# Optimization experiments

Measured on AMD Instinct MI355X. Metric: run time of the kernel, lower is better.

The kernel has to match this reference:

```python
import jax, jax.numpy as jnp
import numpy as np

N_STEPS = 3  # fixed propagation depth standing in for the BFS-guided delta_st recursion


def setup_inputs() -> dict:
    key = jax.random.key(0)
    ks = jax.random.split(key, 12)
    n, d, E = 32, 96, 256
    f32 = jnp.float32
    rn = lambda k, s, sc: jax.random.normal(k, s, f32) * sc
    return {
        "node_embeddings": rn(ks[0], (n, d), 1.0),
        "edges": jax.random.randint(ks[1], (E, 2), 0, n, jnp.int32),
        "w1": rn(ks[2], (4, 4, 3), 0.3), "b1": jnp.full((4,), 0.01, f32),
        "w2": rn(ks[3], (4, 4, 3), 0.3), "b2": jnp.full((4,), 0.01, f32),
        "w3": rn(ks[4], (4, 4, 3), 0.3), "b3": jnp.full((4,), 0.01, f32),
        "fc1_w": rn(ks[5], (16, 128), 0.2), "fc1_b": jnp.full((128,), 0.01, f32),
        "fc2_w": rn(ks[6], (128, 256), 0.1), "fc2_b": jnp.full((256,), 0.01, f32),
        "fc3_w": rn(ks[7], (256, 128), 0.1), "fc3_b": jnp.full((128,), 0.01, f32),
        "fc4_w": rn(ks[8], (128, 1), 0.1), "fc4_b": jnp.full((1,), 0.01, f32),
    }


def _conv1d(x, w, b, stride):
    # x: [B, C, L], w: [O, I, K]
    y = jax.lax.conv_general_dilated(x, w, (stride,), 'VALID',
                                     dimension_numbers=('NCH', 'OIH', 'NCH'))
    return y + b[None, :, None]


def _maxpool2(x):
    return jax.lax.reduce_window(x, -jnp.inf, jax.lax.max, (1, 1, 2), (1, 1, 2), 'VALID')


def _conv_pool_stack(x, w1, b1, w2, b2, w3, b3,
                     fc1_w, fc1_b, fc2_w, fc2_b, fc3_w, fc3_b, fc4_w, fc4_b):
    # x: [B, 4, 96] -> [B]
    h = _maxpool2(jax.nn.relu(_conv1d(x, w1, b1, 2)))   # [B,4,23]
    h = _maxpool2(jax.nn.relu(_conv1d(h, w2, b2, 1)))   # [B,4,10]
    h = _maxpool2(jax.nn.relu(_conv1d(h, w3, b3, 1)))   # [B,4,4]
    h = h.reshape(h.shape[0], -1)                       # [B,16]
    h = jax.nn.relu(h @ fc1_w + fc1_b)
    h = jax.nn.relu(h @ fc2_w + fc2_b)
    h = jax.nn.relu(h @ fc3_w + fc3_b)
    return (h @ fc4_w + fc4_b)[:, 0]


def reference(node_embeddings, edges, w1, b1, w2, b2, w3, b3,
              fc1_w, fc1_b, fc2_w, fc2_b, fc3_w, fc3_b, fc4_w, fc4_b):
    n, d = node_embeddings.shape
    E = edges.shape[0]
    u_idx, v_idx = edges[:, 0], edges[:, 1]

    # All (s, t) node pairs, flattened: P = n*n (s == t masked out below).
    s_idx, t_idx = jnp.meshgrid(jnp.arange(n), jnp.arange(n), indexing='ij')
    s_idx, t_idx = s_idx.reshape(-1), t_idx.reshape(-1)
    P = n * n

    se = node_embeddings[s_idx]  # [P, d]
    te = node_embeddings[t_idx]  # [P, d]
    ue = node_embeddings[u_idx]  # [E, d]
    ve = node_embeddings[v_idx]  # [E, d]

    # stuv input: [P, E, 4, d] -> [P*E, 4, d]
    stuv = jnp.stack([
        jnp.broadcast_to(se[:, None, :], (P, E, d)),
        jnp.broadcast_to(te[:, None, :], (P, E, d)),
        jnp.broadcast_to(ue[None, :, :], (P, E, d)),
        jnp.broadcast_to(ve[None, :, :], (P, E, d)),
    ], axis=2).reshape(P * E, 4, d)

    preds = _conv_pool_stack(stuv, w1, b1, w2, b2, w3, b3,
                             fc1_w, fc1_b, fc2_w, fc2_b,
                             fc3_w, fc3_b, fc4_w, fc4_b).reshape(P, E)

    # zero out s == t pairs (the original skips them)
    preds = preds * (s_idx != t_idx).astype(preds.dtype)[:, None]

    # delta_st: propagate unit mass from s through the per-pair sparse routing
    # matrix R[u, v] = preds[p, e] for N_STEPS hops, accumulating arrivals.
    x = jax.nn.one_hot(s_idx, n, dtype=preds.dtype)  # [P, n]
    rbc = jnp.zeros((n,), preds.dtype)
    for _ in range(N_STEPS):
        gathered = x[:, u_idx] * preds                      # [P, E]
        x = jnp.zeros((P, n), preds.dtype).at[:, v_idx].add(gathered)
        rbc = rbc + x.sum(axis=0)

    return rbc / jnp.sum(rbc)
```

## Files before the change

kernel.cpp:

```cpp
#include <hip/hip_runtime.h>

constexpr int F_ELEMS = 4 * 32 * 4 * 48;
constexpr int PREDS_OFF = F_ELEMS;
constexpr int RBCP_OFF = PREDS_OFF + 1024 * 256;
constexpr int CNT_OFF = RBCP_OFF + 2048;
constexpr int W1P_OFF = CNT_OFF + 16;
constexpr int W2P_OFF = W1P_OFF + 2048;
constexpr int W3P_OFF = W2P_OFF + 16384;

typedef __attribute__((ext_vector_type(8))) short short8;
typedef __attribute__((ext_vector_type(4))) short short4v;
typedef __attribute__((ext_vector_type(4))) float f32x4;

__device__ __forceinline__ unsigned short f2bf(float x) {
    unsigned u = __float_as_uint(x);
    u += 0x7FFF + ((u >> 16) & 1);
    return (unsigned short)(u >> 16);
}

__global__ void prep_all(const float* __restrict__ emb, const float* __restrict__ w1,
                         const float* __restrict__ fc1_w, const float* __restrict__ fc2_w,
                         const float* __restrict__ fc3_w,
                         float* __restrict__ F, unsigned short* __restrict__ W1p,
                         unsigned short* __restrict__ W2p, unsigned short* __restrict__ W3p,
                         float* __restrict__ rbcp_zero) {
    int b = blockIdx.x;
    if (b < 96) {
        int idx = b * 256 + threadIdx.x;
        int i = idx % 48;
        int o = (idx / 48) % 4;
        int node = (idx / 192) % 32;
        int c = idx / 6144;
        float acc = 0.f;
        if (i < 46) {
#pragma unroll
            for (int k = 0; k < 3; k++) acc += w1[(o * 4 + c) * 3 + k] * emb[node * 96 + 2 * i + k];
        }
        F[idx] = acc;
        return;
    }
    if (b < 112) {
        int t = (b - 96) * 256 + threadIdx.x;
        int j = t & 7, lane = (t >> 3) & 63, mt = t >> 9;
        int k = (lane >> 4) * 8 + j, n = mt * 16 + (lane & 15);
        float w = (k < 16) ? fc1_w[k * 128 + n] : 0.f;
        W1p[t] = f2bf(w);
        return;
    }
    if (b < 240) {
        int t = (b - 112) * 256 + threadIdx.x;
        int j = t & 7, lane = (t >> 3) & 63, ks = (t >> 9) & 3, mt = t >> 11;
        int k = ks * 32 + (lane >> 4) * 8 + j, n = mt * 16 + (lane & 15);
        W2p[t] = f2bf(fc2_w[k * 256 + n]);
        return;
    }
    if (b < 368) {
        int t = (b - 240) * 256 + threadIdx.x;
        int j = t & 7, lane = (t >> 3) & 63, ks = (t >> 9) & 7, mt = t >> 12;
        int k = ks * 32 + (lane >> 4) * 8 + j, n = mt * 16 + (lane & 15);
        W3p[t] = f2bf(fc3_w[k * 128 + n]);
        return;
    }
    for (int k = threadIdx.x; k < 2064; k += 256) rbcp_zero[k] = 0.f;
}

__global__ __launch_bounds__(256, 4)
void mlp_kernel(const float* __restrict__ F, const int* __restrict__ edges,
                const float* __restrict__ b1v,
                const float* __restrict__ w2, const float* __restrict__ b2,
                const float* __restrict__ w3, const float* __restrict__ b3,
                const float* __restrict__ fc1_b, const float* __restrict__ fc2_b,
                const float* __restrict__ fc3_b,
                const float* __restrict__ fc4_w, const float* __restrict__ fc4_b,
                const unsigned short* __restrict__ W1p, const unsigned short* __restrict__ W2p,
                const unsigned short* __restrict__ W3p,
                float* __restrict__ preds) {
    __shared__ __align__(16) float smem[8448];
    unsigned short* X1 = (unsigned short*)smem;
    unsigned short* X3h = (unsigned short*)smem;
    unsigned short* X2 = (unsigned short*)(smem + 4096);
    float* part = smem + 8192;

    const int tid = threadIdx.x;
    const int p = blockIdx.x >> 2;
    const int e0 = (blockIdx.x & 3) * 64;
    const int s = p >> 5, t = p & 31;
    if (s == t) return;

    const int gsample = tid >> 2, o = tid & 3;
    float h1[23];
    {
        const int e = e0 + gsample;
        const int u = edges[2 * e], v = edges[2 * e + 1];
        const f32x4* F0 = (const f32x4*)(F + ((0 * 32 + s) * 4 + o) * 48);
        const f32x4* F1 = (const f32x4*)(F + ((1 * 32 + t) * 4 + o) * 48);
        const f32x4* F2 = (const f32x4*)(F + ((2 * 32 + u) * 4 + o) * 48);
        const f32x4* F3 = (const f32x4*)(F + ((3 * 32 + v) * 4 + o) * 48);
        const float bb = b1v[o];
        float pre[46];
#pragma unroll
        for (int q = 0; q < 12; q++) {
            f32x4 x = F0[q] + F1[q] + F2[q] + F3[q];
#pragma unroll
            for (int z = 0; z < 4; z++) {
                int i = 4 * q + z;
                if (i < 46) pre[i] = fmaxf(x[z] + bb, 0.f);
            }
        }
#pragma unroll
        for (int j = 0; j < 23; j++) h1[j] = fmaxf(pre[2 * j], pre[2 * j + 1]);
    }
    float h2[10];
    {
        float wm[4][3];
#pragma unroll
        for (int m = 0; m < 4; m++)
#pragma unroll
            for (int k = 0; k < 3; k++) wm[m][k] = w2[o * 12 + (o ^ m) * 3 + k];
        const float bb = b2[o];
        float win[4][3];
#pragma unroll
        for (int j = 0; j < 2; j++) {
            float x = h1[j];
            win[0][j] = x;
            win[1][j] = __shfl_xor(x, 1, 64);
            win[2][j] = __shfl_xor(x, 2, 64);
            win[3][j] = __shfl_xor(x, 3, 64);
        }
        float pre[20];
#pragma unroll
        for (int i = 0; i < 20; i++) {
            float x = h1[i + 2];
            win[0][(i + 2) % 3] = x;
            win[1][(i + 2) % 3] = __shfl_xor(x, 1, 64);
            win[2][(i + 2) % 3] = __shfl_xor(x, 2, 64);
            win[3][(i + 2) % 3] = __shfl_xor(x, 3, 64);
            float acc = bb;
#pragma unroll
            for (int m = 0; m < 4; m++)
#pragma unroll
                for (int k = 0; k < 3; k++)
                    acc = fmaf(wm[m][k], win[m][(i + k) % 3], acc);
            pre[i] = fmaxf(acc, 0.f);
        }
#pragma unroll
        for (int j = 0; j < 10; j++) h2[j] = fmaxf(pre[2 * j], pre[2 * j + 1]);
    }
    {
        float wm[4][3];
#pragma unroll
        for (int m = 0; m < 4; m++)
#pragma unroll
            for (int k = 0; k < 3; k++) wm[m][k] = w3[o * 12 + (o ^ m) * 3 + k];
        const float bb = b3[o];
        float win[4][3];
#pragma unroll
        for (int j = 0; j < 2; j++) {
            float x = h2[j];
            win[0][j] = x;
            win[1][j] = __shfl_xor(x, 1, 64);
            win[2][j] = __shfl_xor(x, 2, 64);
            win[3][j] = __shfl_xor(x, 3, 64);
        }
        float pre[8];
#pragma unroll
        for (int i = 0; i < 8; i++) {
            float x = h2[i + 2];
            win[0][(i + 2) % 3] = x;
            win[1][(i + 2) % 3] = __shfl_xor(x, 1, 64);
            win[2][(i + 2) % 3] = __shfl_xor(x, 2, 64);
            win[3][(i + 2) % 3] = __shfl_xor(x, 3, 64);
            float acc = bb;
#pragma unroll
            for (int m = 0; m < 4; m++)
#pragma unroll
                for (int k = 0; k < 3; k++)
                    acc = fmaf(wm[m][k], win[m][(i + k) % 3], acc);
            pre[i] = fmaxf(acc, 0.f);
        }
        short4v pk;
#pragma unroll
        for (int l = 0; l < 4; l++)
            pk[l] = (short)f2bf(fmaxf(pre[2 * l], pre[2 * l + 1]));
        *(short4v*)(X1 + (((o >> 1) * 64 + gsample) * 8) + (o & 1) * 4) = pk;
        short4v z4 = (short4v){0, 0, 0, 0};
        *(short4v*)(X1 + ((((o >> 1) + 2) * 64 + gsample) * 8) + (o & 1) * 4) = z4;
    }
    __syncthreads();
    const int lane = tid & 63, wave = tid >> 6;
    const int mrow = lane & 15, quad = lane >> 4;
    {
        const short8* W1v = (const short8*)W1p;
        short8 bnt[4];
#pragma unroll
        for (int nt = 0; nt < 4; nt++)
            bnt[nt] = *(const short8*)(X1 + (quad * 64 + nt * 16 + mrow) * 8);
        f32x4 acc1[2][4];
#pragma unroll
        for (int a = 0; a < 2; a++)
#pragma unroll
            for (int b = 0; b < 4; b++) acc1[a][b] = (f32x4){0.f, 0.f, 0.f, 0.f};
#pragma unroll
        for (int mtl = 0; mtl < 2; mtl++) {
            const int mt = wave * 2 + mtl;
            short8 ah = W1v[mt * 64 + lane];
#pragma unroll
            for (int nt = 0; nt < 4; nt++)
                acc1[mtl][nt] = __builtin_amdgcn_mfma_f32_16x16x32_bf16(ah, bnt[nt], acc1[mtl][nt], 0, 0, 0);
        }
#pragma unroll
        for (int mtl = 0; mtl < 2; mtl++) {
            const int mt = wave * 2 + mtl;
            const int n0 = mt * 16 + quad * 4;
            f32x4 b4 = *(const f32x4*)(fc1_b + n0);
#pragma unroll
            for (int nt = 0; nt < 4; nt++) {
                short4v pk;
#pragma unroll
                for (int r = 0; r < 4; r++)
                    pk[r] = (short)f2bf(fmaxf(acc1[mtl][nt][r] + b4[r], 0.f));
                *(short4v*)(X2 + ((n0 >> 3) * 64 + nt * 16 + mrow) * 8 + (n0 & 7)) = pk;
            }
        }
    }
    __syncthreads();
    const short8* W2v = (const short8*)W2p;
    const short8* W3v = (const short8*)W3p;
    f32x4 acc3[2][4];
#pragma unroll
    for (int a = 0; a < 2; a++)
#pragma unroll
        for (int b = 0; b < 4; b++) acc3[a][b] = (f32x4){0.f, 0.f, 0.f, 0.f};
#pragma unroll
    for (int h = 0; h < 2; h++) {
        f32x4 acc2[2][4];
#pragma unroll
        for (int a = 0; a < 2; a++)
#pragma unroll
            for (int b = 0; b < 4; b++) acc2[a][b] = (f32x4){0.f, 0.f, 0.f, 0.f};
#pragma unroll
        for (int ks = 0; ks < 4; ks++) {
            short8 bfr[4];
#pragma unroll
            for (int nt = 0; nt < 4; nt++)
                bfr[nt] = *(const short8*)(X2 + ((ks * 4 + quad) * 64 + nt * 16 + mrow) * 8);
#pragma unroll
            for (int mtl = 0; mtl < 2; mtl++) {
                const int mt = h * 8 + wave * 2 + mtl;
                short8 ah = W2v[(mt * 4 + ks) * 64 + lane];
#pragma unroll
                for (int nt = 0; nt < 4; nt++)
                    acc2[mtl][nt] = __builtin_amdgcn_mfma_f32_16x16x32_bf16(ah, bfr[nt], acc2[mtl][nt], 0, 0, 0);
            }
        }
#pragma unroll
        for (int mtl = 0; mtl < 2; mtl++) {
            const int mt = h * 8 + wave * 2 + mtl;
            const int n0 = mt * 16 + quad * 4;
            const int kl = n0 - h * 128;
            f32x4 b4 = *(const f32x4*)(fc2_b + n0);
#pragma unroll
            for (int nt = 0; nt < 4; nt++) {
                short4v pk;
#pragma unroll
                for (int r = 0; r < 4; r++)
                    pk[r] = (short)f2bf(fmaxf(acc2[mtl][nt][r] + b4[r], 0.f));
                *(short4v*)(X3h + ((kl >> 3) * 64 + nt * 16 + mrow) * 8 + (kl & 7)) = pk;
            }
        }
        __syncthreads();
#pragma unroll
        for (int ksl = 0; ksl < 4; ksl++) {
            const int ks = h * 4 + ksl;
            short8 bfr[4];
#pragma unroll
            for (int nt = 0; nt < 4; nt++)
                bfr[nt] = *(const short8*)(X3h + ((ksl * 4 + quad) * 64 + nt * 16 + mrow) * 8);
#pragma unroll
            for (int mtl = 0; mtl < 2; mtl++) {
                const int mt = wave * 2 + mtl;
                short8 ah = W3v[(mt * 8 + ks) * 64 + lane];
#pragma unroll
                for (int nt = 0; nt < 4; nt++)
                    acc3[mtl][nt] = __builtin_amdgcn_mfma_f32_16x16x32_bf16(ah, bfr[nt], acc3[mtl][nt], 0, 0, 0);
            }
        }
        __syncthreads();
    }
    {
        float p4[4] = {0.f, 0.f, 0.f, 0.f};
#pragma unroll
        for (int mtl = 0; mtl < 2; mtl++) {
            const int mt = wave * 2 + mtl;
            const int n0 = mt * 16 + quad * 4;
            f32x4 b4 = *(const f32x4*)(fc3_b + n0);
            f32x4 w44 = *(const f32x4*)(fc4_w + n0);
#pragma unroll
            for (int nt = 0; nt < 4; nt++)
#pragma unroll
                for (int r = 0; r < 4; r++)
                    p4[nt] = fmaf(fmaxf(acc3[mtl][nt][r] + b4[r], 0.f), w44[r], p4[nt]);
        }
#pragma unroll
        for (int nt = 0; nt < 4; nt++) {
            p4[nt] += __shfl_xor(p4[nt], 16, 64);
            p4[nt] += __shfl_xor(p4[nt], 32, 64);
        }
        if (quad == 0) {
#pragma unroll
            for (int nt = 0; nt < 4; nt++)
                part[wave * 64 + nt * 16 + mrow] = p4[nt];
        }
    }
    __syncthreads();
    if (tid < 64) {
        float pred = part[tid] + part[64 + tid] + part[128 + tid] + part[192 + tid] + fc4_b[0];
        preds[p * 256 + e0 + tid] = pred;
    }
}

__global__ __launch_bounds__(256)
void prop_norm(const int* __restrict__ edges, const float* __restrict__ preds,
               float* __restrict__ rbc_part, int* __restrict__ counter,
               float* __restrict__ out) {
    const int tid = threadIdx.x;
    const int wave = tid >> 6, lane = tid & 63;
    const int p = blockIdx.x * 4 + wave;
    const int s = p >> 5, t = p & 31;
    __shared__ float xw[4][32], xnw[4][32], raccw[4][32];
    __shared__ float red[8][32];
    __shared__ int lastflag;
    int u[4], v[4];
    float pr[4];
#pragma unroll
    for (int j = 0; j < 4; j++) {
        int e = lane + 64 * j;
        u[j] = edges[2 * e];
        v[j] = edges[2 * e + 1];
        pr[j] = preds[p * 256 + e];
    }
    if (lane < 32) { xw[wave][lane] = (lane == s) ? 1.f : 0.f; raccw[wave][lane] = 0.f; }
    const bool active = (s != t);
    for (int step = 0; step < 3; step++) {
        if (lane < 32) xnw[wave][lane] = 0.f;
        __syncthreads();
        if (active) {
#pragma unroll
            for (int j = 0; j < 4; j++)
                atomicAdd(&xnw[wave][v[j]], xw[wave][u[j]] * pr[j]);
        }
        __syncthreads();
        if (lane < 32) { raccw[wave][lane] += xnw[wave][lane]; xw[wave][lane] = xnw[wave][lane]; }
        __syncthreads();
    }
    if (active && lane < 32) atomicAdd(&rbc_part[(p & 63) * 32 + lane], raccw[wave][lane]);
    __syncthreads();
    if (tid == 0) lastflag = (atomicAdd(counter, 1) == 255);
    __syncthreads();
    if (!lastflag) return;
    const int node = tid & 31, sub = tid >> 5;
    float vv = 0.f;
#pragma unroll
    for (int g = 0; g < 8; g++)
        vv += atomicAdd(&rbc_part[(sub * 8 + g) * 32 + node], 0.f);
    red[sub][node] = vv;
    __syncthreads();
    if (tid < 32) {
        float acc = 0.f;
#pragma unroll
        for (int sb = 0; sb < 8; sb++) acc += red[sb][tid];
        float tot = acc;
#pragma unroll
        for (int mask = 1; mask < 32; mask <<= 1) tot += __shfl_xor(tot, mask, 32);
        out[tid] = acc / tot;
    }
}

extern "C" void kernel_launch(void* const* d_in, const int* in_sizes, int n_in,
                              void* d_out, int out_size, void* d_ws, size_t ws_size,
                              hipStream_t stream) {
    const float* emb = (const float*)d_in[0];
    const int* edges = (const int*)d_in[1];
    const float* w1 = (const float*)d_in[2];
    const float* b1 = (const float*)d_in[3];
    const float* w2 = (const float*)d_in[4];
    const float* b2 = (const float*)d_in[5];
    const float* w3 = (const float*)d_in[6];
    const float* b3 = (const float*)d_in[7];
    const float* fc1_w = (const float*)d_in[8];
    const float* fc1_b = (const float*)d_in[9];
    const float* fc2_w = (const float*)d_in[10];
    const float* fc2_b = (const float*)d_in[11];
    const float* fc3_w = (const float*)d_in[12];
    const float* fc3_b = (const float*)d_in[13];
    const float* fc4_w = (const float*)d_in[14];
    const float* fc4_b = (const float*)d_in[15];

    float* ws = (float*)d_ws;
    float* F = ws;
    float* preds = ws + PREDS_OFF;
    float* rbc_part = ws + RBCP_OFF;
    int* counter = (int*)(ws + CNT_OFF);
    unsigned short* W1p = (unsigned short*)(ws + W1P_OFF);
    unsigned short* W2p = (unsigned short*)(ws + W2P_OFF);
    unsigned short* W3p = (unsigned short*)(ws + W3P_OFF);
    float* out = (float*)d_out;

    prep_all<<<dim3(369), dim3(256), 0, stream>>>(emb, w1, fc1_w, fc2_w, fc3_w,
                                                  F, W1p, W2p, W3p, rbc_part);
    mlp_kernel<<<dim3(4096), dim3(256), 0, stream>>>(
        F, edges, b1, w2, b2, w3, b3, fc1_b, fc2_b, fc3_b,
        fc4_w, fc4_b, W1p, W2p, W3p, preds);
    prop_norm<<<dim3(256), dim3(256), 0, stream>>>(edges, preds, rbc_part, counter, out);
}
```

Before: 167.7 us.

## Fuse propagation kernel into MLP kernel using per-pair completion counters

The separate propagation and normalisation kernel is folded into the MLP kernel as 256 extra trailing blocks. Each of these blocks spin-waits on a per-pair counter until all four edge-chunk blocks for its pair have published their predictions. Predictions are written and read through atomics so they are visible across blocks. This removes one kernel launch and lets propagation overlap the MLP tail. The cost is spin-waiting blocks that hold compute-unit slots, and reliance on block dispatch order to avoid deadlock.

```diff
diff --git a/kernel.cpp b/kernel.cpp
--- a/kernel.cpp
+++ b/kernel.cpp
@@ -4,9 +4,11 @@
 constexpr int PREDS_OFF = F_ELEMS;
 constexpr int RBCP_OFF = PREDS_OFF + 1024 * 256;
 constexpr int CNT_OFF = RBCP_OFF + 2048;
-constexpr int W1P_OFF = CNT_OFF + 16;
+constexpr int PAIRCNT_OFF = CNT_OFF + 16;
+constexpr int W1P_OFF = PAIRCNT_OFF + 1024;
 constexpr int W2P_OFF = W1P_OFF + 2048;
 constexpr int W3P_OFF = W2P_OFF + 16384;
+constexpr int ZERO_LEN = 2048 + 16 + 1024;
 
 typedef __attribute__((ext_vector_type(8))) short short8;
 typedef __attribute__((ext_vector_type(4))) short short4v;
@@ -61,7 +63,7 @@
         W3p[t] = f2bf(fc3_w[k * 128 + n]);
         return;
     }
-    for (int k = threadIdx.x; k < 2064; k += 256) rbcp_zero[k] = 0.f;
+    for (int k = threadIdx.x; k < ZERO_LEN; k += 256) rbcp_zero[k] = 0.f;
 }
 
 __global__ __launch_bounds__(256, 4)
@@ -74,14 +76,86 @@
                 const float* __restrict__ fc4_w, const float* __restrict__ fc4_b,
                 const unsigned short* __restrict__ W1p, const unsigned short* __restrict__ W2p,
                 const unsigned short* __restrict__ W3p,
-                float* __restrict__ preds) {
+                float* __restrict__ preds, float* __restrict__ rbc_part,
+                int* __restrict__ pair_cnt, int* __restrict__ gcnt,
+                float* __restrict__ out) {
     __shared__ __align__(16) float smem[8448];
+    const int tid = threadIdx.x;
+
+    if (blockIdx.x >= 4096) {
+        const int bidx = blockIdx.x - 4096;
+        const int wave = tid >> 6, lane = tid & 63;
+        const int p = bidx * 4 + wave;
+        const int s = p >> 5, t = p & 31;
+        float* xw = smem;
+        float* xnw = smem + 128;
+        float* raccw = smem + 256;
+        float* red = smem + 384;
+        __shared__ int lastflag;
+        const bool active = (s != t);
+        if (active) {
+            int cnt = 0;
+            do {
+                if (lane == 0) cnt = atomicAdd(&pair_cnt[p], 0);
+                cnt = __shfl(cnt, 0, 64);
+                if (cnt < 4) __builtin_amdgcn_s_sleep(8);
+            } while (cnt < 4);
+        }
+        int u[4], v[4];
+        float pr[4];
+#pragma unroll
+        for (int j = 0; j < 4; j++) {
+            int e = lane + 64 * j;
+            u[j] = edges[2 * e];
+            v[j] = edges[2 * e + 1];
+            pr[j] = active ? atomicAdd(&preds[p * 256 + e], 0.f) : 0.f;
+        }
+        if (lane < 32) { xw[wave * 32 + lane] = (lane == s) ? 1.f : 0.f; raccw[wave * 32 + lane] = 0.f; }
+        for (int step = 0; step < 3; step++) {
+            if (lane < 32) xnw[wave * 32 + lane] = 0.f;
+            __syncthreads();
+            if (active) {
+#pragma unroll
+                for (int j = 0; j < 4; j++)
+                    atomicAdd(&xnw[wave * 32 + v[j]], xw[wave * 32 + u[j]] * pr[j]);
+            }
+            __syncthreads();
+            if (lane < 32) {
+                raccw[wave * 32 + lane] += xnw[wave * 32 + lane];
+                xw[wave * 32 + lane] = xnw[wave * 32 + lane];
+            }
+            __syncthreads();
+        }
+        if (active && lane < 32) atomicAdd(&rbc_part[(p & 63) * 32 + lane], raccw[wave * 32 + lane]);
+        __syncthreads();
+        if (tid == 0) lastflag = (atomicAdd(gcnt, 1) == 255);
+        __syncthreads();
+        if (!lastflag) return;
+        const int node = tid & 31, sub = tid >> 5;
+        float vv = 0.f;
+#pragma unroll
+        for (int g = 0; g < 8; g++)
+            vv += atomicAdd(&rbc_part[(sub * 8 + g) * 32 + node], 0.f);
+        __syncthreads();
+        red[sub * 32 + node] = vv;
+        __syncthreads();
+        if (tid < 32) {
+            float acc = 0.f;
+#pragma unroll
+            for (int sb = 0; sb < 8; sb++) acc += red[sb * 32 + tid];
+            float tot = acc;
+#pragma unroll
+            for (int mask = 1; mask < 32; mask <<= 1) tot += __shfl_xor(tot, mask, 32);
+            out[tid] = acc / tot;
+        }
+        return;
+    }
+
     unsigned short* X1 = (unsigned short*)smem;
     unsigned short* X3h = (unsigned short*)smem;
     unsigned short* X2 = (unsigned short*)(smem + 4096);
     float* part = smem + 8192;
 
-    const int tid = threadIdx.x;
     const int p = blockIdx.x >> 2;
     const int e0 = (blockIdx.x & 3) * 64;
     const int s = p >> 5, t = p & 31;
@@ -315,65 +389,10 @@
     __syncthreads();
     if (tid < 64) {
         float pred = part[tid] + part[64 + tid] + part[128 + tid] + part[192 + tid] + fc4_b[0];
-        preds[p * 256 + e0 + tid] = pred;
-    }
-}
-
-__global__ __launch_bounds__(256)
-void prop_norm(const int* __restrict__ edges, const float* __restrict__ preds,
-               float* __restrict__ rbc_part, int* __restrict__ counter,
-               float* __restrict__ out) {
-    const int tid = threadIdx.x;
-    const int wave = tid >> 6, lane = tid & 63;
-    const int p = blockIdx.x * 4 + wave;
-    const int s = p >> 5, t = p & 31;
-    __shared__ float xw[4][32], xnw[4][32], raccw[4][32];
-    __shared__ float red[8][32];
-    __shared__ int lastflag;
-    int u[4], v[4];
-    float pr[4];
-#pragma unroll
-    for (int j = 0; j < 4; j++) {
-        int e = lane + 64 * j;
-        u[j] = edges[2 * e];
-        v[j] = edges[2 * e + 1];
-        pr[j] = preds[p * 256 + e];
-    }
-    if (lane < 32) { xw[wave][lane] = (lane == s) ? 1.f : 0.f; raccw[wave][lane] = 0.f; }
-    const bool active = (s != t);
-    for (int step = 0; step < 3; step++) {
-        if (lane < 32) xnw[wave][lane] = 0.f;
-        __syncthreads();
-        if (active) {
-#pragma unroll
-            for (int j = 0; j < 4; j++)
-                atomicAdd(&xnw[wave][v[j]], xw[wave][u[j]] * pr[j]);
-        }
-        __syncthreads();
-        if (lane < 32) { raccw[wave][lane] += xnw[wave][lane]; xw[wave][lane] = xnw[wave][lane]; }
-        __syncthreads();
-    }
-    if (active && lane < 32) atomicAdd(&rbc_part[(p & 63) * 32 + lane], raccw[wave][lane]);
+        atomicExch(&preds[p * 256 + e0 + tid], pred);
+    }
     __syncthreads();
-    if (tid == 0) lastflag = (atomicAdd(counter, 1) == 255);
-    __syncthreads();
-    if (!lastflag) return;
-    const int node = tid & 31, sub = tid >> 5;
-    float vv = 0.f;
-#pragma unroll
-    for (int g = 0; g < 8; g++)
-        vv += atomicAdd(&rbc_part[(sub * 8 + g) * 32 + node], 0.f);
-    red[sub][node] = vv;
-    __syncthreads();
-    if (tid < 32) {
-        float acc = 0.f;
-#pragma unroll
-        for (int sb = 0; sb < 8; sb++) acc += red[sb][tid];
-        float tot = acc;
-#pragma unroll
-        for (int mask = 1; mask < 32; mask <<= 1) tot += __shfl_xor(tot, mask, 32);
-        out[tid] = acc / tot;
-    }
+    if (tid == 0) atomicAdd(&pair_cnt[p], 1);
 }
 
 extern "C" void kernel_launch(void* const* d_in, const int* in_sizes, int n_in,
@@ -400,7 +419,8 @@
     float* F = ws;
     float* preds = ws + PREDS_OFF;
     float* rbc_part = ws + RBCP_OFF;
-    int* counter = (int*)(ws + CNT_OFF);
+    int* gcnt = (int*)(ws + CNT_OFF);
+    int* pair_cnt = (int*)(ws + PAIRCNT_OFF);
     unsigned short* W1p = (unsigned short*)(ws + W1P_OFF);
     unsigned short* W2p = (unsigned short*)(ws + W2P_OFF);
     unsigned short* W3p = (unsigned short*)(ws + W3P_OFF);
@@ -408,8 +428,7 @@
 
     prep_all<<<dim3(369), dim3(256), 0, stream>>>(emb, w1, fc1_w, fc2_w, fc3_w,
                                                   F, W1p, W2p, W3p, rbc_part);
-    mlp_kernel<<<dim3(4096), dim3(256), 0, stream>>>(
+    mlp_kernel<<<dim3(4352), dim3(256), 0, stream>>>(
         F, edges, b1, w2, b2, w3, b3, fc1_b, fc2_b, fc3_b,
-        fc4_w, fc4_b, W1p, W2p, W3p, preds);
-    prop_norm<<<dim3(256), dim3(256), 0, stream>>>(edges, preds, rbc_part, counter, out);
+        fc4_w, fc4_b, W1p, W2p, W3p, preds, rbc_part, pair_cnt, gcnt, out);
 }
```

Result: slower. 176.1 us (+5.0%).
